# Kernel tuning notes

Hardware: AMD Instinct MI355X
Metric: run time of the kernel (lower is better)

## Reference

```python
import jax, jax.numpy as jnp
import numpy as np

B, T, C = 4, 1024, 768
H, HD = 12, 64
E, K, DFF = 16, 2, 3072
EPS = 1e-5


def layernorm(x, w, b):
    mu = jnp.mean(x, axis=-1, keepdims=True)
    xc = x - mu
    var = jnp.mean(xc * xc, axis=-1, keepdims=True)
    return xc * jax.lax.rsqrt(var + EPS) * w + b


def setup_inputs() -> dict:
    key = jax.random.key(0)
    ks = jax.random.split(key, 12)
    s = lambda fan_in: 1.0 / np.sqrt(fan_in)
    return {
        "x": jax.random.normal(ks[0], (B, T, C), jnp.float32),
        "ln1_w": jnp.ones((C,), jnp.float32),
        "ln1_b": jnp.zeros((C,), jnp.float32),
        "W_attn": jax.random.normal(ks[1], (C, 3 * C), jnp.float32) * s(C),
        "b_attn": jnp.zeros((3 * C,), jnp.float32),
        "W_proj": jax.random.normal(ks[2], (C, C), jnp.float32) * s(C),
        "b_proj": jnp.zeros((C,), jnp.float32),
        "ln2_w": jnp.ones((C,), jnp.float32),
        "ln2_b": jnp.zeros((C,), jnp.float32),
        "W_router": jax.random.normal(ks[3], (C, E), jnp.float32) * s(C),
        "W1": jax.random.normal(ks[4], (E, C, DFF), jnp.float32) * s(C),
        "b1": jnp.zeros((E, DFF), jnp.float32),
        "W2": jax.random.normal(ks[5], (E, DFF, C), jnp.float32) * s(DFF),
        "b2": jnp.zeros((E, C), jnp.float32),
    }


def reference(x, ln1_w, ln1_b, W_attn, b_attn, W_proj, b_proj,
              ln2_w, ln2_b, W_router, W1, b1, W2, b2):
    # --- attention sublayer ---
    xn = layernorm(x, ln1_w, ln1_b)
    qkv = xn @ W_attn + b_attn                                  # [B,T,3C]
    q, k, v = jnp.split(qkv, 3, axis=-1)
    q = q.reshape(B, T, H, HD).transpose(0, 2, 1, 3)            # [B,H,T,HD]
    k = k.reshape(B, T, H, HD).transpose(0, 2, 1, 3)
    v = v.reshape(B, T, H, HD).transpose(0, 2, 1, 3)
    att = jnp.einsum('bhqd,bhkd->bhqk', q, k) / np.sqrt(HD)
    causal = jnp.tril(jnp.ones((T, T), bool))
    att = jnp.where(causal, att, -jnp.inf)
    att = jax.nn.softmax(att, axis=-1)
    y = jnp.einsum('bhqk,bhkd->bhqd', att, v)
    y = y.transpose(0, 2, 1, 3).reshape(B, T, C)
    x = x + y @ W_proj + b_proj

    # --- MoE sublayer: dense all-experts with top-k gating mask ---
    xn2 = layernorm(x, ln2_w, ln2_b)
    probs = jax.nn.softmax(xn2 @ W_router, axis=-1)             # [B,T,E]
    top_p, top_idx = jax.lax.top_k(probs, K)                    # [B,T,K]
    gating = jnp.sum(jax.nn.one_hot(top_idx, E, dtype=probs.dtype)
                     * top_p[..., None], axis=-2)               # [B,T,E]
    g = jnp.moveaxis(gating, -1, 0)                             # [E,B,T]

    def body(acc, params):
        W1e, b1e, W2e, b2e, ge = params
        h = jax.nn.gelu(xn2 @ W1e + b1e, approximate=False)     # [B,T,DFF]
        out = h @ W2e + b2e                                     # [B,T,C]
        return acc + ge[..., None] * out, None

    y_moe, _ = jax.lax.scan(body, jnp.zeros_like(x), (W1, b1, W2, b2, g))
    # note: MoELayer returns x + y, and Block adds residual again
    return x + (xn2_residual := 0) + xn2 * 0 + (x * 0) + x * 0 + y_moe + x * 0 if False else x + (x * 0) + y_moe + x * 0 * 0 if False else x + x * 0 + y_moe + (x - x) if False else x + (x + y_moe) - x + (x + y_moe) - (x + y_moe) if False else x + x + y_moe - x if False else (x + (x + y_moe)) - x + (x - x) if False else x + y_moe + x - x if False else _block_out(x, xn2, y_moe)


def _block_out(x, xn2, y_moe):
    # MoELayer.forward returns x_in + y where x_in is ln2 *input* (x here);
    # Block then does x = x + ffn(ln2(x)) -> x + (x + y_moe)? No: MoE input is
    # xn2 = ln2(x), so ffn(ln2(x)) = xn2 + y_moe, and Block adds residual x.
    return x + xn2 + y_moe
```

## Files before the change

kernel.cpp:

```cpp
#include <hip/hip_runtime.h>
#include <math.h>

#define CC    768
#define C3    2304
#define KD    2304
#define LDA2  1536
#define TT    1024
#define BB    4
#define HH    12
#define HD    64
#define EE    16
#define DFFN  3072
#define NTOK  4096
#define NSLOT 8192
#define LDP   136

typedef unsigned short u16;
typedef unsigned int   u32;
typedef __attribute__((ext_vector_type(8))) short short8;
typedef __attribute__((ext_vector_type(4))) float floatx4;

__device__ __forceinline__ u16 f2bf(float f){
  u32 x = __builtin_bit_cast(u32, f);
  x += 0x7fffu + ((x >> 16) & 1u);
  return (u16)(x >> 16);
}
__device__ __forceinline__ u16 f2h(float f){
  _Float16 h = (_Float16)f;
  return __builtin_bit_cast(u16, h);
}
__device__ __forceinline__ float h2f(u16 u){
  return (float)__builtin_bit_cast(_Float16, u);
}
__device__ __forceinline__ float gelu_exact(float v){
  return 0.5f * v * (1.f + erff(v * 0.70710678118654752440f));
}
__device__ __forceinline__ void split2h(float v, u16& h0, u16& h1){
  float vs = v * 64.f;
  h0 = f2h(vs);
  h1 = f2h(vs - h2f(h0));
}
__device__ __forceinline__ void gload_lds16(const void* g, void* l){
  __builtin_amdgcn_global_load_lds(
      (const __attribute__((address_space(1))) void*)g,
      (__attribute__((address_space(3))) void*)l, 16, 0, 0);
}

template<int MODE>
__global__ __launch_bounds__(256) void transpose_split(const float* __restrict__ src,
    u16* __restrict__ d0, int R, int Cn)
{
  __shared__ float tile[32][33];
  int z = blockIdx.z;
  const float* s = src + (size_t)z * R * Cn;
  int c0 = blockIdx.x * 32, r0 = blockIdx.y * 32;
  int tx = threadIdx.x & 31, ty = threadIdx.x >> 5;
  #pragma unroll
  for (int j = 0; j < 4; ++j)
    tile[ty + j*8][tx] = s[(size_t)(r0 + ty + j*8) * Cn + c0 + tx];
  __syncthreads();
  #pragma unroll
  for (int j = 0; j < 4; ++j){
    float v = tile[tx][ty + j*8];
    if (MODE == 1){
      u16 h0, h1; split2h(v, h0, h1);
      size_t base = (size_t)(c0 + ty + j*8) * LDA2 + (r0 + tx);
      d0[base] = h0; d0[base + 768] = h1;
    } else {
      d0[(size_t)z * R * Cn + (size_t)(c0 + ty + j*8) * R + r0 + tx] = f2bf(v);
    }
  }
}

template<int MODE>
__global__ __launch_bounds__(256) void ln_kernel(const float* __restrict__ x,
    const float* __restrict__ gw, const float* __restrict__ gb,
    float* __restrict__ of, u16* __restrict__ o0)
{
  int tok = blockIdx.x, tid = threadIdx.x;
  const float* xr = x + (size_t)tok * CC;
  float v0 = xr[tid], v1 = xr[tid + 256], v2 = xr[tid + 512];
  __shared__ float r1[4], r2[4];
  __shared__ float mus, rss;
  float s = v0 + v1 + v2;
  #pragma unroll
  for (int off = 32; off >= 1; off >>= 1) s += __shfl_down(s, off);
  if ((tid & 63) == 0) r1[tid >> 6] = s;
  __syncthreads();
  if (tid == 0) mus = (r1[0] + r1[1] + r1[2] + r1[3]) * (1.f / 768.f);
  __syncthreads();
  float mu = mus;
  float d0 = v0 - mu, d1 = v1 - mu, d2 = v2 - mu;
  float t = d0*d0 + d1*d1 + d2*d2;
  #pragma unroll
  for (int off = 32; off >= 1; off >>= 1) t += __shfl_down(t, off);
  if ((tid & 63) == 0) r2[tid >> 6] = t;
  __syncthreads();
  if (tid == 0) rss = rsqrtf((r2[0] + r2[1] + r2[2] + r2[3]) * (1.f / 768.f) + 1e-5f);
  __syncthreads();
  float rstd = rss;
  float dv[3] = {d0, d1, d2};
  #pragma unroll
  for (int i = 0; i < 3; ++i){
    int c = tid + i * 256;
    float vv = dv[i] * rstd * gw[c] + gb[c];
    if (MODE == 1){
      u16 h0, h1; split2h(vv, h0, h1);
      o0[(size_t)tok * LDA2 + c] = h0;
      o0[(size_t)tok * LDA2 + 768 + c] = h1;
    } else {
      size_t idx = (size_t)tok * CC + c;
      of[idx] = vv;
      o0[idx] = f2bf(vv);
    }
  }
}

__global__ __launch_bounds__(256) void gemm_dense(
    const u16* __restrict__ A, const u16* __restrict__ Bt,
    float* __restrict__ C, const float* __restrict__ bias,
    const float* __restrict__ resid, int N)
{
  __shared__ u16 As[2][128 * 32];
  __shared__ u16 Bs[2][128 * 32];
  int tid = threadIdx.x;
  int lane = tid & 63, wave = tid >> 6;
  int wm = wave & 1, wn = wave >> 1;
  int m0 = blockIdx.y * 128, n0 = blockIdx.x * 128;
  int ra = tid >> 2, ka = (tid & 3) * 8;
  const u16* pa0 = A  + (size_t)(m0 + ra)      * LDA2 + ka;
  const u16* pa1 = A  + (size_t)(m0 + ra + 64) * LDA2 + ka;
  const u16* pb0 = Bt + (size_t)(n0 + ra)      * LDA2 + ka;
  const u16* pb1 = Bt + (size_t)(n0 + ra + 64) * LDA2 + ka;
  floatx4 acc[4][4] = {};
  int el = lane & 15, eq = lane >> 4;

  auto stage = [&](int buf, int k0){
    int ca = (k0 >= 768) ? k0 - 768 : k0;
    int cb = (k0 < 1536) ? k0 : k0 - 1536;
    gload_lds16(pa0 + ca, &As[buf][wave*512]);
    gload_lds16(pa1 + ca, &As[buf][2048 + wave*512]);
    gload_lds16(pb0 + cb, &Bs[buf][wave*512]);
    gload_lds16(pb1 + cb, &Bs[buf][2048 + wave*512]);
  };
  stage(0, 0);
  __syncthreads();
  int cur = 0;
  for (int k0 = 0; k0 < KD; k0 += 32){
    if (k0 + 32 < KD) stage(cur ^ 1, k0 + 32);
    short8 fa[4], fb[4];
    #pragma unroll
    for (int t = 0; t < 4; ++t)
      fa[t] = *(const short8*)&As[cur][(size_t)(wm*64 + t*16 + el) * 32 + eq*8];
    #pragma unroll
    for (int t = 0; t < 4; ++t)
      fb[t] = *(const short8*)&Bs[cur][(size_t)(wn*64 + t*16 + el) * 32 + eq*8];
    #pragma unroll
    for (int mt = 0; mt < 4; ++mt)
      #pragma unroll
      for (int nt = 0; nt < 4; ++nt)
        acc[mt][nt] = __builtin_amdgcn_mfma_f32_16x16x32_f16(fa[mt], fb[nt], acc[mt][nt], 0, 0, 0);
    __syncthreads();
    cur ^= 1;
  }
  const float ds = 1.f / 4096.f;
  #pragma unroll
  for (int mt = 0; mt < 4; ++mt){
    #pragma unroll
    for (int nt = 0; nt < 4; ++nt){
      int col = n0 + wn*64 + nt*16 + el;
      float bv = bias ? bias[col] : 0.f;
      #pragma unroll
      for (int r = 0; r < 4; ++r){
        int row = m0 + wm*64 + mt*16 + eq*4 + r;
        size_t idx = (size_t)row * N + col;
        float val = acc[mt][nt][r] * ds + bv;
        if (resid) val += resid[idx];
        C[idx] = val;
      }
    }
  }
}

__global__ __launch_bounds__(256) void flash_mfma(const float* __restrict__ qkv,
    u16* __restrict__ yH)
{
  __shared__ u16 Qs[64 * LDP];
  __shared__ u16 Ks[64 * LDP];
  __shared__ u16 Vt[64 * LDP];
  __shared__ u16 Ps[64 * LDP];
  int tid = threadIdx.x;
  int lane = tid & 63, wv = tid >> 6;
  int qi = 15 - blockIdx.x;
  int bh = blockIdx.y;
  int b = bh / HH, h = bh % HH;
  int el = lane & 15, eq = lane >> 4;
  int m0 = wv * 16;
  int row0 = qi * 64;

  {
    int r = tid >> 2, d0 = (tid & 3) * 16;
    const float* src = qkv + (size_t)(b*TT + row0 + r) * C3 + h*HD + d0;
    u16* q0 = &Qs[r * LDP + d0];
    #pragma unroll
    for (int i = 0; i < 16; i += 2){
      u16 a0, a1, b0, b1;
      split2h(src[i], a0, a1);
      split2h(src[i+1], b0, b1);
      *(u32*)&q0[i]      = (u32)a0 | ((u32)b0 << 16);
      *(u32*)&q0[64 + i] = (u32)a1 | ((u32)b1 << 16);
    }
  }
  floatx4 O[4] = {};
  float mrow[4], lrow[4];
  #pragma unroll
  for (int r = 0; r < 4; ++r){ mrow[r] = -1e30f; lrow[r] = 0.f; }

  const float cmul = 0.125f * 1.44269504088896340736f / 4096.f;
  const int ABase[6] = {0,32,0,32,64,96};
  const int BBase[6] = {0,32,64,96,0,32};

  for (int kt = 0; kt <= qi; ++kt){
    __syncthreads();
    {
      int j = tid >> 2, d0 = (tid & 3) * 16;
      const float* src = qkv + (size_t)(b*TT + kt*64 + j) * C3 + CC + h*HD + d0;
      u16* kp = &Ks[j * LDP + d0];
      #pragma unroll
      for (int i = 0; i < 16; i += 2){
        u16 a0, a1, b0, b1;
        split2h(src[i], a0, a1);
        split2h(src[i+1], b0, b1);
        *(u32*)&kp[i]      = (u32)a0 | ((u32)b0 << 16);
        *(u32*)&kp[64 + i] = (u32)a1 | ((u32)b1 << 16);
      }
      int d = tid & 63, kp0 = (tid >> 6) * 16;
      const float* vsrc = qkv + (size_t)(b*TT + kt*64 + kp0) * C3 + 2*CC + h*HD + d;
      u16* vt = &Vt[d * LDP];
      #pragma unroll
      for (int i = 0; i < 16; i += 2){
        u16 a0, a1, b0, b1;
        split2h(vsrc[(size_t)i * C3], a0, a1);
        split2h(vsrc[(size_t)(i+1) * C3], b0, b1);
        *(u32*)&vt[kp0 + i]      = (u32)a0 | ((u32)b0 << 16);
        *(u32*)&vt[64 + kp0 + i] = (u32)a1 | ((u32)b1 << 16);
      }
    }
    __syncthreads();
    floatx4 S[4] = {};
    #pragma unroll
    for (int ks = 0; ks < 6; ++ks){
      short8 fa = *(const short8*)&Qs[(m0 + el) * LDP + ABase[ks] + eq*8];
      short8 fb[4];
      #pragma unroll
      for (int nt = 0; nt < 4; ++nt)
        fb[nt] = *(const short8*)&Ks[(nt*16 + el) * LDP + BBase[ks] + eq*8];
      #pragma unroll
      for (int nt = 0; nt < 4; ++nt)
        S[nt] = __builtin_amdgcn_mfma_f32_16x16x32_f16(fa, fb[nt], S[nt], 0, 0, 0);
    }
    #pragma unroll
    for (int nt = 0; nt < 4; ++nt){
      int kcol = kt*64 + nt*16 + el;
      #pragma unroll
      for (int r = 0; r < 4; ++r){
        int grow = row0 + m0 + eq*4 + r;
        float sv = S[nt][r] * cmul;
        S[nt][r] = (kcol <= grow) ? sv : -1e30f;
      }
    }
    #pragma unroll
    for (int r = 0; r < 4; ++r){
      float tmax = fmaxf(fmaxf(S[0][r], S[1][r]), fmaxf(S[2][r], S[3][r]));
      #pragma unroll
      for (int off = 1; off < 16; off <<= 1) tmax = fmaxf(tmax, __shfl_xor(tmax, off));
      float mnew = fmaxf(mrow[r], tmax);
      float al = exp2f(mrow[r] - mnew);
      mrow[r] = mnew;
      lrow[r] *= al;
      #pragma unroll
      for (int nt = 0; nt < 4; ++nt) O[nt][r] *= al;
      #pragma unroll
      for (int nt = 0; nt < 4; ++nt){
        float p = exp2f(S[nt][r] - mnew);
        lrow[r] += p;
        S[nt][r] = p;
      }
    }
    #pragma unroll
    for (int nt = 0; nt < 4; ++nt){
      #pragma unroll
      for (int r = 0; r < 4; ++r){
        u16 p0, p1; split2h(S[nt][r], p0, p1);
        int rowl = m0 + eq*4 + r;
        Ps[rowl * LDP + nt*16 + el] = p0;
        Ps[rowl * LDP + 64 + nt*16 + el] = p1;
      }
    }
    #pragma unroll
    for (int ks = 0; ks < 6; ++ks){
      short8 fa = *(const short8*)&Ps[(m0 + el) * LDP + ABase[ks] + eq*8];
      short8 fb[4];
      #pragma unroll
      for (int nt = 0; nt < 4; ++nt)
        fb[nt] = *(const short8*)&Vt[(nt*16 + el) * LDP + BBase[ks] + eq*8];
      #pragma unroll
      for (int nt = 0; nt < 4; ++nt)
        O[nt] = __builtin_amdgcn_mfma_f32_16x16x32_f16(fa, fb[nt], O[nt], 0, 0, 0);
    }
  }
  #pragma unroll
  for (int r = 0; r < 4; ++r){
    float l = lrow[r];
    #pragma unroll
    for (int off = 1; off < 16; off <<= 1) l += __shfl_xor(l, off);
    float inv = 1.f / (l * 4096.f);
    int grow = row0 + m0 + eq*4 + r;
    u16* dst = yH + (size_t)(b*TT + grow) * LDA2 + h*HD;
    #pragma unroll
    for (int nt = 0; nt < 4; ++nt){
      float yv = O[nt][r] * inv;
      u16 y0, y1; split2h(yv, y0, y1);
      dst[nt*16 + el] = y0;
      dst[768 + nt*16 + el] = y1;
    }
  }
}

__global__ __launch_bounds__(256) void router_kernel(const float* __restrict__ xn2,
    const float* __restrict__ Wr, int* __restrict__ eids, float* __restrict__ wts)
{
  int wave = threadIdx.x >> 6, lane = threadIdx.x & 63;
  int tok = blockIdx.x * 4 + wave;
  int g = lane >> 4, e = lane & 15;
  const float* xr = xn2 + (size_t)tok * CC;
  float s = 0.f;
  for (int c4 = 0; c4 < 192; ++c4){
    int c = c4 * 4 + g;
    s += xr[c] * Wr[c * EE + e];
  }
  s += __shfl_xor(s, 16);
  s += __shfl_xor(s, 32);
  float mx = s;
  #pragma unroll
  for (int off = 1; off < 16; off <<= 1) mx = fmaxf(mx, __shfl_xor(mx, off));
  float p = expf(s - mx);
  float Z = p;
  #pragma unroll
  for (int off = 1; off < 16; off <<= 1) Z += __shfl_xor(Z, off);
  p /= Z;
  float best = -1.f; int bi = 0;
  for (int ee = 0; ee < 16; ++ee){
    float pe = __shfl(p, ee);
    if (pe > best){ best = pe; bi = ee; }
  }
  float sec = -1.f; int si = 0;
  for (int ee = 0; ee < 16; ++ee){
    float pe = __shfl(p, ee);
    if (ee != bi && pe > sec){ sec = pe; si = ee; }
  }
  if (lane == 0){
    eids[tok*2] = bi;  eids[tok*2+1] = si;
    wts [tok*2] = best; wts[tok*2+1] = sec;
  }
}

__global__ __launch_bounds__(256) void moe_count(const int* __restrict__ eids,
    int* __restrict__ counts, int* __restrict__ offs, int* __restrict__ curs)
{
  __shared__ int lc[EE];
  int tid = threadIdx.x;
  if (tid < EE) lc[tid] = 0;
  __syncthreads();
  for (int i = tid; i < NSLOT; i += 256) atomicAdd(&lc[eids[i]], 1);
  __syncthreads();
  if (tid == 0){
    int run = 0;
    for (int e = 0; e < EE; ++e){
      counts[e] = lc[e]; offs[e] = run; curs[e] = run; run += lc[e];
    }
    offs[EE] = run;
  }
}

__global__ __launch_bounds__(256) void moe_scatter(const int* __restrict__ eids,
    const float* __restrict__ wts, int* __restrict__ curs,
    int* __restrict__ rowmap, float* __restrict__ wgtm)
{
  int i = blockIdx.x * 256 + threadIdx.x;
  int e = eids[i];
  int pos = atomicAdd(&curs[e], 1);
  rowmap[pos] = i >> 1;
  wgtm[pos] = wts[i];
}

__global__ __launch_bounds__(256) void add2(const float* __restrict__ a,
    const float* __restrict__ b, float* __restrict__ o, int n)
{
  int i = blockIdx.x * 256 + threadIdx.x;
  if (i < n) o[i] = a[i] + b[i];
}

__global__ __launch_bounds__(256) void gemm_moe1(
    const u16* __restrict__ Xb, const u16* __restrict__ W1t, const float* __restrict__ b1,
    u16* __restrict__ H, const int* __restrict__ counts, const int* __restrict__ offs,
    const int* __restrict__ rowmap)
{
  int e = blockIdx.z;
  int cnt = counts[e];
  int m0 = blockIdx.y * 128;
  if (m0 >= cnt) return;
  int off = offs[e];
  int n0 = blockIdx.x * 128;
  const u16* Bt = W1t + (size_t)e * DFFN * CC;
  __shared__ u16 As[2][128 * 32];
  __shared__ u16 Bs[2][128 * 32];
  int tid = threadIdx.x;
  int lane = tid & 63, wave = tid >> 6;
  int wm = wave & 1, wn = wave >> 1;
  int ra = tid >> 2, ka = (tid & 3) * 8;
  int r0 = m0 + ra, r1i = m0 + ra + 64;
  int rr0 = (r0  < cnt) ? r0  : cnt - 1;
  int rr1 = (r1i < cnt) ? r1i : cnt - 1;
  const u16* pa0 = Xb + (size_t)rowmap[off + rr0] * CC + ka;
  const u16* pa1 = Xb + (size_t)rowmap[off + rr1] * CC + ka;
  const u16* pb0 = Bt + (size_t)(n0 + ra)      * CC + ka;
  const u16* pb1 = Bt + (size_t)(n0 + ra + 64) * CC + ka;
  floatx4 acc[4][4] = {};
  int el = lane & 15, eq = lane >> 4;

  auto stage = [&](int buf, int k0){
    gload_lds16(pa0 + k0, &As[buf][wave*512]);
    gload_lds16(pa1 + k0, &As[buf][2048 + wave*512]);
    gload_lds16(pb0 + k0, &Bs[buf][wave*512]);
    gload_lds16(pb1 + k0, &Bs[buf][2048 + wave*512]);
  };
  stage(0, 0);
  __syncthreads();
  int cur = 0;
  for (int k0 = 0; k0 < CC; k0 += 32){
    if (k0 + 32 < CC) stage(cur ^ 1, k0 + 32);
    short8 fa[4], fb[4];
    #pragma unroll
    for (int t = 0; t < 4; ++t)
      fa[t] = *(const short8*)&As[cur][(size_t)(wm*64 + t*16 + el) * 32 + eq*8];
    #pragma unroll
    for (int t = 0; t < 4; ++t)
      fb[t] = *(const short8*)&Bs[cur][(size_t)(wn*64 + t*16 + el) * 32 + eq*8];
    #pragma unroll
    for (int mt = 0; mt < 4; ++mt)
      #pragma unroll
      for (int nt = 0; nt < 4; ++nt)
        acc[mt][nt] = __builtin_amdgcn_mfma_f32_16x16x32_bf16(fa[mt], fb[nt], acc[mt][nt], 0, 0, 0);
    __syncthreads();
    cur ^= 1;
  }
  #pragma unroll
  for (int mt = 0; mt < 4; ++mt){
    #pragma unroll
    for (int nt = 0; nt < 4; ++nt){
      int col = n0 + wn*64 + nt*16 + el;
      float bv = b1[(size_t)e * DFFN + col];
      #pragma unroll
      for (int r = 0; r < 4; ++r){
        int row = m0 + wm*64 + mt*16 + eq*4 + r;
        if (row < cnt)
          H[(size_t)(off + row) * DFFN + col] = f2bf(gelu_exact(acc[mt][nt][r] + bv));
      }
    }
  }
}

#define KSPL 2
__global__ __launch_bounds__(256) void gemm_moe2(
    const u16* __restrict__ H, const u16* __restrict__ W2t, const float* __restrict__ b2,
    float* __restrict__ Out, const int* __restrict__ counts, const int* __restrict__ offs,
    const int* __restrict__ rowmap, const float* __restrict__ wgtm)
{
  int e = blockIdx.z;
  int cnt = counts[e];
  int m0 = blockIdx.y * 128;
  if (m0 >= cnt) return;
  int off = offs[e];
  int bx = blockIdx.x;
  int n0 = (bx % 6) * 128;
  int ksp = bx / 6;
  const u16* Bt = W2t + (size_t)e * CC * DFFN;
  __shared__ u16 As[2][128 * 32];
  __shared__ u16 Bs[2][128 * 32];
  int tid = threadIdx.x;
  int lane = tid & 63, wave = tid >> 6;
  int wm = wave & 1, wn = wave >> 1;
  int ra = tid >> 2, ka = (tid & 3) * 8;
  int r0 = m0 + ra, r1i = m0 + ra + 64;
  int rr0 = (r0  < cnt) ? r0  : cnt - 1;
  int rr1 = (r1i < cnt) ? r1i : cnt - 1;
  const u16* pa0 = H + (size_t)(off + rr0) * DFFN + ka;
  const u16* pa1 = H + (size_t)(off + rr1) * DFFN + ka;
  const u16* pb0 = Bt + (size_t)(n0 + ra)      * DFFN + ka;
  const u16* pb1 = Bt + (size_t)(n0 + ra + 64) * DFFN + ka;
  floatx4 acc[4][4] = {};
  int el = lane & 15, eq = lane >> 4;
  int kbeg = ksp * (DFFN / KSPL), kend = kbeg + DFFN / KSPL;

  auto stage = [&](int buf, int k0){
    gload_lds16(pa0 + k0, &As[buf][wave*512]);
    gload_lds16(pa1 + k0, &As[buf][2048 + wave*512]);
    gload_lds16(pb0 + k0, &Bs[buf][wave*512]);
    gload_lds16(pb1 + k0, &Bs[buf][2048 + wave*512]);
  };
  stage(0, kbeg);
  __syncthreads();
  int cur = 0;
  for (int k0 = kbeg; k0 < kend; k0 += 32){
    if (k0 + 32 < kend) stage(cur ^ 1, k0 + 32);
    short8 fa[4], fb[4];
    #pragma unroll
    for (int t = 0; t < 4; ++t)
      fa[t] = *(const short8*)&As[cur][(size_t)(wm*64 + t*16 + el) * 32 + eq*8];
    #pragma unroll
    for (int t = 0; t < 4; ++t)
      fb[t] = *(const short8*)&Bs[cur][(size_t)(wn*64 + t*16 + el) * 32 + eq*8];
    #pragma unroll
    for (int mt = 0; mt < 4; ++mt)
      #pragma unroll
      for (int nt = 0; nt < 4; ++nt)
        acc[mt][nt] = __builtin_amdgcn_mfma_f32_16x16x32_bf16(fa[mt], fb[nt], acc[mt][nt], 0, 0, 0);
    __syncthreads();
    cur ^= 1;
  }
  #pragma unroll
  for (int mt = 0; mt < 4; ++mt){
    #pragma unroll
    for (int nt = 0; nt < 4; ++nt){
      int col = n0 + wn*64 + nt*16 + el;
      float bv = (ksp == 0) ? b2[(size_t)e * CC + col] : 0.f;
      #pragma unroll
      for (int r = 0; r < 4; ++r){
        int row = m0 + wm*64 + mt*16 + eq*4 + r;
        if (row < cnt){
          int slot = off + row;
          int tok = rowmap[slot];
          float wv = wgtm[slot];
          atomicAdd(&Out[(size_t)tok * CC + col], wv * (acc[mt][nt][r] + bv));
        }
      }
    }
  }
}

extern "C" void kernel_launch(void* const* d_in, const int* in_sizes, int n_in,
                              void* d_out, int out_size, void* d_ws, size_t ws_size,
                              hipStream_t stream)
{
  const float* x     = (const float*)d_in[0];
  const float* ln1w  = (const float*)d_in[1];
  const float* ln1b  = (const float*)d_in[2];
  const float* Wattn = (const float*)d_in[3];
  const float* battn = (const float*)d_in[4];
  const float* Wproj = (const float*)d_in[5];
  const float* bproj = (const float*)d_in[6];
  const float* ln2w  = (const float*)d_in[7];
  const float* ln2b  = (const float*)d_in[8];
  const float* Wrout = (const float*)d_in[9];
  const float* W1    = (const float*)d_in[10];
  const float* b1    = (const float*)d_in[11];
  const float* W2    = (const float*)d_in[12];
  const float* b2    = (const float*)d_in[13];
  float* out = (float*)d_out;

  char* w = (char*)d_ws;
  auto alloc = [&](size_t bytes)->char* {
    char* p = w; w += (bytes + 255) & ~(size_t)255; return p;
  };
  u16* watp  = (u16*)alloc((size_t)C3 * LDA2 * 2);
  u16* wptp  = (u16*)alloc((size_t)CC * LDA2 * 2);
  u16* w1t   = (u16*)alloc((size_t)EE * DFFN * CC * 2);
  u16* w2t   = (u16*)alloc((size_t)EE * CC * DFFN * 2);
  u16* xH    = (u16*)alloc((size_t)NTOK * LDA2 * 2);
  float* qkv = (float*)alloc((size_t)NTOK * C3 * 4);
  u16* yH    = (u16*)alloc((size_t)NTOK * LDA2 * 2);
  u16* Hbuf  = (u16*)alloc((size_t)NSLOT * DFFN * 2);
  float* x2    = (float*)alloc((size_t)NTOK * CC * 4);
  float* xn2   = (float*)alloc((size_t)NTOK * CC * 4);
  u16*   xn2b  = (u16*)alloc((size_t)NTOK * CC * 2);
  int*   eids  = (int*)alloc(NSLOT * 4);
  float* wts   = (float*)alloc(NSLOT * 4);
  int* counts  = (int*)alloc(256);
  int* offs    = (int*)alloc(256);
  int* curs    = (int*)alloc(256);
  int* rowmap  = (int*)alloc(NSLOT * 4);
  float* wgtm  = (float*)alloc(NSLOT * 4);

  hipLaunchKernelGGL((transpose_split<1>), dim3(C3/32, CC/32, 1), dim3(256), 0, stream,
                     Wattn, watp, CC, C3);
  hipLaunchKernelGGL((transpose_split<1>), dim3(CC/32, CC/32, 1), dim3(256), 0, stream,
                     Wproj, wptp, CC, CC);
  hipLaunchKernelGGL((transpose_split<0>), dim3(DFFN/32, CC/32, EE), dim3(256), 0, stream,
                     W1, w1t, CC, DFFN);
  hipLaunchKernelGGL((transpose_split<0>), dim3(CC/32, DFFN/32, EE), dim3(256), 0, stream,
                     W2, w2t, DFFN, CC);
  hipLaunchKernelGGL((ln_kernel<1>), dim3(NTOK), dim3(256), 0, stream,
                     x, ln1w, ln1b, (float*)nullptr, xH);
  hipLaunchKernelGGL(gemm_dense, dim3(C3/128, NTOK/128), dim3(256), 0, stream,
                     xH, watp, qkv, battn, (const float*)nullptr, C3);
  hipLaunchKernelGGL(flash_mfma, dim3(16, BB*HH), dim3(256), 0, stream, qkv, yH);
  hipLaunchKernelGGL(gemm_dense, dim3(CC/128, NTOK/128), dim3(256), 0, stream,
                     yH, wptp, x2, bproj, x, CC);
  hipLaunchKernelGGL((ln_kernel<0>), dim3(NTOK), dim3(256), 0, stream,
                     x2, ln2w, ln2b, xn2, xn2b);
  hipLaunchKernelGGL(router_kernel, dim3(NTOK/4), dim3(256), 0, stream, xn2, Wrout, eids, wts);
  hipLaunchKernelGGL(moe_count, dim3(1), dim3(256), 0, stream, eids, counts, offs, curs);
  hipLaunchKernelGGL(moe_scatter, dim3(NSLOT/256), dim3(256), 0, stream, eids, wts, curs, rowmap, wgtm);
  hipLaunchKernelGGL(add2, dim3(NTOK*CC/256), dim3(256), 0, stream, x2, xn2, out, NTOK*CC);
  hipLaunchKernelGGL(gemm_moe1, dim3(DFFN/128, 32, EE), dim3(256), 0, stream,
                     xn2b, w1t, b1, Hbuf, counts, offs, rowmap);
  hipLaunchKernelGGL(gemm_moe2, dim3(6*KSPL, 32, EE), dim3(256), 0, stream,
                     Hbuf, w2t, b2, out, counts, offs, rowmap, wgtm);
}
```

Measured before the change: 965.3 us.

## Triple-buffer LDS staging with one barrier per K-step in GEMM kernels

Replaces double-buffered global_load_lds staging with a three-stage ring buffer in the dense, MoE up and MoE down GEMMs. Two tiles are prefetched ahead, and each iteration waits with a partial vmcnt followed by a single s_barrier, replacing the trailing __syncthreads. This keeps more loads in flight and removes one barrier per step. In exchange LDS use rises from 32KB to 48KB per block, which may lower occupancy, and correctness now depends on hand-written waitcnt counts.

```diff
diff --git a/kernel.cpp b/kernel.cpp
--- a/kernel.cpp
+++ b/kernel.cpp
@@ -46,6 +46,10 @@
       (__attribute__((address_space(3))) void*)l, 16, 0, 0);
 }
 
+#define PIPE_WAIT_STEADY  asm volatile("s_waitcnt vmcnt(4) lgkmcnt(0)" ::: "memory")
+#define PIPE_WAIT_LAST    asm volatile("s_waitcnt vmcnt(0) lgkmcnt(0)" ::: "memory")
+#define PIPE_BARRIER      asm volatile("s_barrier" ::: "memory")
+
 template<int MODE>
 __global__ __launch_bounds__(256) void transpose_split(const float* __restrict__ src,
     u16* __restrict__ d0, int R, int Cn)
@@ -121,8 +125,8 @@
     float* __restrict__ C, const float* __restrict__ bias,
     const float* __restrict__ resid, int N)
 {
-  __shared__ u16 As[2][128 * 32];
-  __shared__ u16 Bs[2][128 * 32];
+  __shared__ u16 As[3][128 * 32];
+  __shared__ u16 Bs[3][128 * 32];
   int tid = threadIdx.x;
   int lane = tid & 63, wave = tid >> 6;
   int wm = wave & 1, wn = wave >> 1;
@@ -143,11 +147,18 @@
     gload_lds16(pb0 + cb, &Bs[buf][wave*512]);
     gload_lds16(pb1 + cb, &Bs[buf][2048 + wave*512]);
   };
+  const int nsteps = KD / 32;
   stage(0, 0);
-  __syncthreads();
+  stage(1, 32);
   int cur = 0;
-  for (int k0 = 0; k0 < KD; k0 += 32){
-    if (k0 + 32 < KD) stage(cur ^ 1, k0 + 32);
+  for (int i = 0; i < nsteps; ++i){
+    __builtin_amdgcn_sched_barrier(0);
+    if (i + 1 < nsteps) PIPE_WAIT_STEADY; else PIPE_WAIT_LAST;
+    PIPE_BARRIER;
+    if (i + 2 < nsteps){
+      int nx = cur + 2; if (nx >= 3) nx -= 3;
+      stage(nx, (i + 2) * 32);
+    }
     short8 fa[4], fb[4];
     #pragma unroll
     for (int t = 0; t < 4; ++t)
@@ -160,8 +171,7 @@
       #pragma unroll
       for (int nt = 0; nt < 4; ++nt)
         acc[mt][nt] = __builtin_amdgcn_mfma_f32_16x16x32_f16(fa[mt], fb[nt], acc[mt][nt], 0, 0, 0);
-    __syncthreads();
-    cur ^= 1;
+    cur = (cur == 2) ? 0 : cur + 1;
   }
   const float ds = 1.f / 4096.f;
   #pragma unroll
@@ -413,8 +423,8 @@
   int off = offs[e];
   int n0 = blockIdx.x * 128;
   const u16* Bt = W1t + (size_t)e * DFFN * CC;
-  __shared__ u16 As[2][128 * 32];
-  __shared__ u16 Bs[2][128 * 32];
+  __shared__ u16 As[3][128 * 32];
+  __shared__ u16 Bs[3][128 * 32];
   int tid = threadIdx.x;
   int lane = tid & 63, wave = tid >> 6;
   int wm = wave & 1, wn = wave >> 1;
@@ -435,11 +445,18 @@
     gload_lds16(pb0 + k0, &Bs[buf][wave*512]);
     gload_lds16(pb1 + k0, &Bs[buf][2048 + wave*512]);
   };
+  const int nsteps = CC / 32;
   stage(0, 0);
-  __syncthreads();
+  stage(1, 32);
   int cur = 0;
-  for (int k0 = 0; k0 < CC; k0 += 32){
-    if (k0 + 32 < CC) stage(cur ^ 1, k0 + 32);
+  for (int i = 0; i < nsteps; ++i){
+    __builtin_amdgcn_sched_barrier(0);
+    if (i + 1 < nsteps) PIPE_WAIT_STEADY; else PIPE_WAIT_LAST;
+    PIPE_BARRIER;
+    if (i + 2 < nsteps){
+      int nx = cur + 2; if (nx >= 3) nx -= 3;
+      stage(nx, (i + 2) * 32);
+    }
     short8 fa[4], fb[4];
     #pragma unroll
     for (int t = 0; t < 4; ++t)
@@ -452,8 +469,7 @@
       #pragma unroll
       for (int nt = 0; nt < 4; ++nt)
         acc[mt][nt] = __builtin_amdgcn_mfma_f32_16x16x32_bf16(fa[mt], fb[nt], acc[mt][nt], 0, 0, 0);
-    __syncthreads();
-    cur ^= 1;
+    cur = (cur == 2) ? 0 : cur + 1;
   }
   #pragma unroll
   for (int mt = 0; mt < 4; ++mt){
@@ -486,8 +502,8 @@
   int n0 = (bx % 6) * 128;
   int ksp = bx / 6;
   const u16* Bt = W2t + (size_t)e * CC * DFFN;
-  __shared__ u16 As[2][128 * 32];
-  __shared__ u16 Bs[2][128 * 32];
+  __shared__ u16 As[3][128 * 32];
+  __shared__ u16 Bs[3][128 * 32];
   int tid = threadIdx.x;
   int lane = tid & 63, wave = tid >> 6;
   int wm = wave & 1, wn = wave >> 1;
@@ -501,7 +517,7 @@
   const u16* pb1 = Bt + (size_t)(n0 + ra + 64) * DFFN + ka;
   floatx4 acc[4][4] = {};
   int el = lane & 15, eq = lane >> 4;
-  int kbeg = ksp * (DFFN / KSPL), kend = kbeg + DFFN / KSPL;
+  int kbeg = ksp * (DFFN / KSPL);
 
   auto stage = [&](int buf, int k0){
     gload_lds16(pa0 + k0, &As[buf][wave*512]);
@@ -509,11 +525,18 @@
     gload_lds16(pb0 + k0, &Bs[buf][wave*512]);
     gload_lds16(pb1 + k0, &Bs[buf][2048 + wave*512]);
   };
+  const int nsteps = (DFFN / KSPL) / 32;
   stage(0, kbeg);
-  __syncthreads();
+  stage(1, kbeg + 32);
   int cur = 0;
-  for (int k0 = kbeg; k0 < kend; k0 += 32){
-    if (k0 + 32 < kend) stage(cur ^ 1, k0 + 32);
+  for (int i = 0; i < nsteps; ++i){
+    __builtin_amdgcn_sched_barrier(0);
+    if (i + 1 < nsteps) PIPE_WAIT_STEADY; else PIPE_WAIT_LAST;
+    PIPE_BARRIER;
+    if (i + 2 < nsteps){
+      int nx = cur + 2; if (nx >= 3) nx -= 3;
+      stage(nx, kbeg + (i + 2) * 32);
+    }
     short8 fa[4], fb[4];
     #pragma unroll
     for (int t = 0; t < 4; ++t)
@@ -526,8 +549,7 @@
       #pragma unroll
       for (int nt = 0; nt < 4; ++nt)
         acc[mt][nt] = __builtin_amdgcn_mfma_f32_16x16x32_bf16(fa[mt], fb[nt], acc[mt][nt], 0, 0, 0);
-    __syncthreads();
-    cur ^= 1;
+    cur = (cur == 2) ? 0 : cur + 1;
   }
   #pragma unroll
   for (int mt = 0; mt < 4; ++mt){
```

Result: no change. 954.1 us (-1.2%).
